# Kernel optimization log

Hardware: AMD Instinct MI355X
Metric: run time of the kernel (lower is better)

Reference implementation:

```python
import jax, jax.numpy as jnp
import numpy as np

N_FILTERS = 64
FILTER_SIZE = 64
N_FRAMES = 64
N_TO_KEEP = 128
MIN_SIZE = 512
N_SAMPLES = 32768
BATCH = 8


def pos_encoding(n_elements, n_sinusoids):
    t = np.linspace(1e-8, 1.0, n_elements)
    freq = np.linspace(1e-3, 1.0, n_sinusoids)
    return np.sin(t[:, None] * freq[None, :]).astype(np.float32)


def gammatone_filter_bank(n_filters, size, sr=22050.0):
    # 4th-order gammatone impulse responses, linearly spaced center freqs
    t = np.arange(size) / sr
    freqs = np.linspace(20.0, sr / 2 - 20.0, n_filters)
    b = 1.019 * 24.7 * (4.37 * freqs / 1000.0 + 1.0)  # ERB bandwidths
    g = (t[None, :] ** 3) * np.exp(-2 * np.pi * b[:, None] * t[None, :]) \
        * np.cos(2 * np.pi * freqs[:, None] * t[None, :])
    g = g / (np.abs(g).max(axis=-1, keepdims=True) + 1e-12)
    return g.astype(np.float32)


def setup_inputs() -> dict:
    key = jax.random.key(0)
    k1, k2 = jax.random.split(key)
    return {
        'target': jax.random.normal(k1, (BATCH, 1, N_SAMPLES), dtype=jnp.float32),
        'recon': jax.random.normal(k2, (BATCH, 1, N_SAMPLES), dtype=jnp.float32),
        'filters': jnp.asarray(gammatone_filter_bank(N_FILTERS, FILTER_SIZE)),
        'proj_time': jnp.asarray(pos_encoding(N_FRAMES, 128)),
        'proj_freq': jnp.asarray(pos_encoding(N_FILTERS, 128)),
    }


def fft_frequency_decompose(x, min_size):
    # band-limited octave decomposition: band of size s holds rfft bins [s/4, s/2)
    coeffs = jnp.fft.rfft(x, norm='ortho')
    n = x.shape[-1]
    bands = []
    start, end = 0, min_size // 2
    while end <= n // 2:
        spec = jnp.zeros(x.shape[:-1] + (end + 1,), dtype=coeffs.dtype)
        spec = spec.at[..., start:end].set(coeffs[..., start:end])
        bands.append(jnp.fft.irfft(spec, n=end * 2, norm='ortho'))
        start, end = end, end * 2
    return bands


def fft_convolve(a, b):
    n = a.shape[-1]
    pa = jnp.pad(a, [(0, 0)] * (a.ndim - 1) + [(0, n)])
    pb = jnp.pad(b, [(0, 0)] * (b.ndim - 1) + [(0, n)])
    spec = jnp.fft.rfft(pa) * jnp.fft.rfft(pb)  # broadcasts [B,1,.] x [1,F,.]
    return jnp.fft.irfft(spec, n=2 * n)[..., :n]


def max_pool1d(x, kernel, stride, pad):
    return jax.lax.reduce_window(
        x, -jnp.inf, jax.lax.max,
        (1, 1, kernel), (1, 1, stride),
        [(0, 0), (0, 0), (pad, pad)])


def sparsify2(x, k):
    # top-k over flattened (channels*time); pack events as value-scaled time
    # one-hots and binary channel one-hots
    b, c, t = x.shape
    flat = x.reshape(b, c * t)
    values, indices = jax.lax.top_k(flat, k)  # [b, k]
    ch, tm = indices // t, indices % t
    packed = (tm[..., None] == jnp.arange(t)[None, None, :]).astype(x.dtype) * values[..., None]  # [b,k,t]
    one_hot = (ch[..., None] == jnp.arange(c)[None, None, :]).astype(x.dtype)  # [b,k,c]
    return packed, one_hot


def _feature(x, filters, proj_time, proj_freq):
    bands = fft_frequency_decompose(x, MIN_SIZE)
    outs = []
    for band in bands:  # fixed small set of structurally distinct bands
        samples = band.shape[-1]
        filt = jnp.pad(filters[None, :, :], ((0, 0), (0, 0), (0, samples - FILTER_SIZE)))
        result = fft_convolve(band, filt)  # [B, n_filters, samples]
        stride = samples // 64
        pooled = max_pool1d(result, 2 * stride, stride, stride // 2)[..., :samples]  # [B, 64, 64]
        packed, one_hot = sparsify2(pooled, N_TO_KEEP)
        a = packed @ proj_time   # [B, k, 128]
        b = one_hot @ proj_freq  # [B, k, 128]
        outs.append(jnp.concatenate([a, b], axis=-1))
    return jnp.concatenate(outs, axis=-1)  # [B, k, 256 * n_bands]


def reference(target, recon, filters, proj_time, proj_freq):
    t = _feature(target, filters, proj_time, proj_freq)
    r = _feature(recon, filters, proj_time, proj_freq)
    return jnp.abs(t - r).mean()
```

## Files before the change

### kernel.cpp

```cpp
#include <hip/hip_runtime.h>
#include <hip/hip_bf16.h>

#define N_SAMP    32768
#define NBINS     16384
#define NSIG      16
#define NBANDS    7
#define K_TOP     128
#define BAND_STRIDE 65472

#define SST_F   0
#define SST_PT  4096
#define SST_PF  12288
#define SST_TOT 20480

#define TWO_PI 6.283185307179586f

typedef __attribute__((ext_vector_type(8))) short bf16x8;
typedef __attribute__((ext_vector_type(4))) float f32x4;

__device__ __forceinline__ float bf2f(__hip_bfloat16 v) { return __bfloat162float(v); }

__device__ __forceinline__ unsigned encf(float f) {
    unsigned u = __float_as_uint(f);
    return (u & 0x80000000u) ? ~u : (u | 0x80000000u);
}
__device__ __forceinline__ float decf(unsigned u) {
    return __uint_as_float((u & 0x80000000u) ? (u ^ 0x80000000u) : ~u);
}

__device__ __forceinline__ int band_M1sh(int b) { return b < 3 ? 4 : (b < 4 ? 5 : 6); }
__device__ __forceinline__ int band_Lsh(int b) {
    return b == 0 ? 5 : (b == 1 ? 6 : (b < 5 ? 7 : (b == 5 ? 8 : 9)));
}
__device__ __forceinline__ int band_M2sh(int b) {
    return b < 2 ? 4 : (b < 5 ? 5 : (b == 5 ? 6 : 7));
}

__global__ __launch_bounds__(256) void k_fwd1(
    const void* __restrict__ tgt, const void* __restrict__ rec,
    const void* __restrict__ f, const void* __restrict__ pt,
    const void* __restrict__ pf,
    __hip_bfloat16* __restrict__ staged,
    float* __restrict__ bands, float* __restrict__ accum,
    int* __restrict__ counter,
    float* __restrict__ T)
{
    const int tid   = threadIdx.x;
    const int sig   = blockIdx.y;

    if (blockIdx.x == 8) {
        float pv0 = bf2f(((const __hip_bfloat16*)tgt)[tid & 63]);
        int bad0 = (fabsf(pv0) > 1e8f) || (pv0 != pv0);
        const int isf = (__ballot(bad0) != 0ull);
        #pragma unroll
        for (int k = 0; k < 5; ++k) {
            int id = sig * 1280 + k * 256 + tid;
            const void* src; int idx;
            if (id < SST_PT)      { src = f;  idx = id; }
            else if (id < SST_PF) { src = pt; idx = id - SST_PT; }
            else                  { src = pf; idx = id - SST_PF; }
            float v = isf ? ((const float*)src)[idx]
                          : bf2f(((const __hip_bfloat16*)src)[idx]);
            staged[id] = __float2bfloat16(v);
        }
        for (int i = tid; i < 448; i += 256) {
            int g = i >> 6, j = i & 63;
            int off = 64 * g + 512 * ((1 << g) - 1);
            bands[(size_t)sig * BAND_STRIDE + off + j] = 0.f;
        }
        if (sig == 0 && tid == 0) { accum[0] = 0.f; counter[0] = 0; }
        return;
    }

    const int nbase = (blockIdx.x & 1) * 128;
    const int kgrp  = ((blockIdx.x >> 1) & 1) * 64;
    const int nqh   = (blockIdx.x >> 2) & 1;
    __shared__ __align__(16) __hip_bfloat16 xT[64][136];
    __shared__ float ct[128], st[128];
    __shared__ float2 t256[256];
    __shared__ float2 tF[128];

    {
        float sv, cv;
        sincosf(TWO_PI * (float)tid * (1.f / 256.f), &sv, &cv);
        t256[tid] = make_float2(cv, -sv);
        if (tid < 128) {
            sincosf(TWO_PI * (float)tid * (1.f / 128.f), &sv, &cv);
            ct[tid] = cv; st[tid] = sv;
            sincosf(TWO_PI * (float)tid * (1.f / 32768.f), &sv, &cv);
            tF[tid] = make_float2(cv, -sv);
        }
    }

    float pv = bf2f(((const __hip_bfloat16*)tgt)[tid & 63]);
    int bad = (fabsf(pv) > 1e8f) || (pv != pv);
    const int isf32 = (__ballot(bad) != 0ull);
    const void* xsrc = (sig < 8) ? tgt : rec;
    const int soff = (sig & 7) * N_SAMP;

    const int rloc = tid & 63;
    const int chb  = (tid >> 6) * 32;
    for (int c8 = 0; c8 < 32; c8 += 8) {
        union { bf16x8 v; __hip_bfloat16 h[8]; } u;
        #pragma unroll
        for (int uu = 0; uu < 8; ++uu) {
            int n1 = chb + c8 + uu;
            int gi = soff + n1 * 256 + nbase + nqh * 64 + rloc;
            float xv = isf32 ? ((const float*)xsrc)[gi]
                             : bf2f(((const __hip_bfloat16*)xsrc)[gi]);
            u.h[uu] = __float2bfloat16(xv);
        }
        *(bf16x8*)(&xT[rloc][chb + c8]) = u.v;
    }
    __syncthreads();

    const int tl = tid & 15, quad = (tid >> 4) & 3, w = tid >> 6;
    const int k1 = kgrp + w * 16 + tl;
    bf16x8 Arh[4], Arl[4], Aih[4], Ail[4];
    #pragma unroll
    for (int ki = 0; ki < 4; ++ki) {
        union { bf16x8 v; __hip_bfloat16 h[8]; } rh, rl, ih, il;
        #pragma unroll
        for (int j = 0; j < 8; ++j) {
            int n1 = ki * 32 + quad * 8 + j;
            int tt = (k1 * n1) & 127;
            float wre = ct[tt], wim = -st[tt];
            __hip_bfloat16 h1 = __float2bfloat16(wre);
            rh.h[j] = h1;
            rl.h[j] = __float2bfloat16(wre - bf2f(h1));
            __hip_bfloat16 h2 = __float2bfloat16(wim);
            ih.h[j] = h2;
            il.h[j] = __float2bfloat16(wim - bf2f(h2));
        }
        Arh[ki] = rh.v; Arl[ki] = rl.v; Aih[ki] = ih.v; Ail[ki] = il.v;
    }

    float2* To = (float2*)T + (size_t)sig * 128 * 256;
    const int mk = kgrp + w * 16 + quad * 4;
    for (int ni = 0; ni < 4; ++ni) {
        bf16x8 B[4];
        #pragma unroll
        for (int ki = 0; ki < 4; ++ki)
            B[ki] = *(const bf16x8*)(&xT[ni * 16 + tl][ki * 32 + quad * 8]);
        f32x4 aR = {0.f,0.f,0.f,0.f}, aI = {0.f,0.f,0.f,0.f};
        #pragma unroll
        for (int ki = 0; ki < 4; ++ki) {
            aR = __builtin_amdgcn_mfma_f32_16x16x32_bf16(Arh[ki], B[ki], aR, 0, 0, 0);
            aR = __builtin_amdgcn_mfma_f32_16x16x32_bf16(Arl[ki], B[ki], aR, 0, 0, 0);
            aI = __builtin_amdgcn_mfma_f32_16x16x32_bf16(Aih[ki], B[ki], aI, 0, 0, 0);
            aI = __builtin_amdgcn_mfma_f32_16x16x32_bf16(Ail[ki], B[ki], aI, 0, 0, 0);
        }
        const int n2 = nbase + nqh * 64 + ni * 16 + tl;
        #pragma unroll
        for (int rg = 0; rg < 4; ++rg) {
            int k1e = mk + rg;
            int m = k1e * n2;
            float2 e1 = t256[m >> 7];
            float2 e2 = tF[m & 127];
            float er = e1.x * e2.x - e1.y * e2.y;
            float ei = e1.x * e2.y + e1.y * e2.x;
            float Tr = aR[rg] * er - aI[rg] * ei;
            float Ti = aI[rg] * er + aR[rg] * ei;
            To[(size_t)k1e * 256 + n2] = make_float2(Tr, Ti);
        }
    }
}

__global__ __launch_bounds__(128) void k_fwd2(
    const float* __restrict__ T, float* __restrict__ C)
{
    const int k2  = threadIdx.x;
    const int k1  = blockIdx.x;
    const int sig = blockIdx.y;
    __shared__ float2 Ts[256];
    __shared__ float2 tw[256];
    const float2* Tin = (const float2*)T + ((size_t)sig * 128 + k1) * 256;
    for (int i = k2; i < 256; i += 128) Ts[i] = Tin[i];
    {
        float sv, cv;
        sincosf(TWO_PI * (float)k2 * (1.f / 256.f), &sv, &cv);
        tw[k2]       = make_float2(cv, -sv);
        tw[k2 + 128] = make_float2(-cv, sv);
    }
    __syncthreads();
    float er[4], ei[4];
    #pragma unroll
    for (int c = 0; c < 4; ++c) {
        float2 e = tw[(c * k2) & 255];
        er[c] = e.x; ei[c] = e.y;
    }
    float2 e4 = tw[(4 * k2) & 255];
    const float c4 = e4.x, s4 = e4.y;
    float Xr[4] = {0.f,0.f,0.f,0.f}, Xi[4] = {0.f,0.f,0.f,0.f};
    for (int n2 = 0; n2 < 256; n2 += 4) {
        #pragma unroll
        for (int c = 0; c < 4; ++c) {
            float2 t = Ts[n2 + c];
            Xr[c] += t.x * er[c] - t.y * ei[c];
            Xi[c] += t.x * ei[c] + t.y * er[c];
            float nr = er[c] * c4 - ei[c] * s4;
            ei[c]    = er[c] * s4 + ei[c] * c4;
            er[c] = nr;
        }
    }
    const float inv = 5.5242717280199030e-3f;
    float xr = (Xr[0] + Xr[1]) + (Xr[2] + Xr[3]);
    float xi = (Xi[0] + Xi[1]) + (Xi[2] + Xi[3]);
    float2* Co = (float2*)C + (size_t)sig * NBINS;
    Co[k1 + 128 * k2] = make_float2(xr * inv, xi * inv);
}

__global__ __launch_bounds__(256) void k_synthA(
    const float* __restrict__ C, float* __restrict__ G)
{
    const int tid = threadIdx.x;
    const int sig = blockIdx.y;
    const int bix = 63 - blockIdx.x;
    const int band = (bix == 0) ? 0 : (32 - __clz(bix));
    const int lbx  = (band == 0) ? 0 : (bix - (1 << (band - 1)));
    const int s    = 512 << band;
    const int m1sh = band_M1sh(band);
    const int lsh  = band_Lsh(band);
    const int m2sh = band_M2sh(band);
    const int M2   = 1 << m2sh;
    const int L    = 1 << lsh;
    const int L4   = L >> 2;
    const int a    = (band == 0) ? 0 : (128 << band);
    const int tix  = lbx * 256 + tid;
    const int j1lo = (lbx * 256) >> (lsh - 2);
    int j1cnt = 256 >> (lsh - 2);
    if (j1cnt > (1 << m1sh)) j1cnt = 1 << m1sh;
    __shared__ float2 Ds[256];
    const float2* D = (const float2*)C + (size_t)sig * NBINS + a;
    for (int i = tid; i < (j1cnt << m2sh); i += 256) {
        int j1o = i >> m2sh, j2 = i & (M2 - 1);
        Ds[i] = D[(j1lo + j1o) + (j2 << m1sh)];
    }
    __syncthreads();
    if (tix >= (128 << band)) return;
    const int j1o = (tix >> (lsh - 2)) - j1lo;
    const int m   = tix & (L4 - 1);
    const float2* Dj = Ds + (j1o << m2sh);
    float e0r = 1.f, e0i = 0.f, e1r, e1i, sr, si;
    sincosf(TWO_PI * (float)m / (float)L, &e1i, &e1r);
    sincosf(TWO_PI * (float)(2 * m) / (float)L, &si, &sr);
    float ar[4] = {0.f,0.f,0.f,0.f}, ai[4] = {0.f,0.f,0.f,0.f};
    for (int j2 = 0; j2 < M2; j2 += 4) {
        {   float2 d = Dj[j2];
            float tr = d.x * e0r - d.y * e0i, ti = d.x * e0i + d.y * e0r;
            ar[0] += tr; ai[0] += ti; ar[1] += tr; ai[1] += ti;
            ar[2] += tr; ai[2] += ti; ar[3] += tr; ai[3] += ti;
            float nr = e0r * sr - e0i * si; e0i = e0r * si + e0i * sr; e0r = nr;
        }
        {   float2 d = Dj[j2 + 1];
            float tr = d.x * e1r - d.y * e1i, ti = d.x * e1i + d.y * e1r;
            ar[0] += tr; ai[0] += ti;
            ar[1] -= ti; ai[1] += tr;
            ar[2] -= tr; ai[2] -= ti;
            ar[3] += ti; ai[3] -= tr;
            float nr = e1r * sr - e1i * si; e1i = e1r * si + e1i * sr; e1r = nr;
        }
        {   float2 d = Dj[j2 + 2];
            float tr = d.x * e0r - d.y * e0i, ti = d.x * e0i + d.y * e0r;
            ar[0] += tr; ai[0] += ti;
            ar[1] -= tr; ai[1] -= ti;
            ar[2] += tr; ai[2] += ti;
            ar[3] -= tr; ai[3] -= ti;
            float nr = e0r * sr - e0i * si; e0i = e0r * si + e0i * sr; e0r = nr;
        }
        {   float2 d = Dj[j2 + 3];
            float tr = d.x * e1r - d.y * e1i, ti = d.x * e1i + d.y * e1r;
            ar[0] += tr; ai[0] += ti;
            ar[1] += ti; ai[1] -= tr;
            ar[2] -= tr; ai[2] -= ti;
            ar[3] -= ti; ai[3] += tr;
            float nr = e1r * sr - e1i * si; e1i = e1r * si + e1i * sr; e1r = nr;
        }
    }
    const float sc = 2.f * rsqrtf((float)s);
    float2* Go = (float2*)G + (size_t)sig * 65024 + 512 * ((1 << band) - 1);
    const int base = ((tix >> (lsh - 2)) << lsh) + m;
    #pragma unroll
    for (int q = 0; q < 4; ++q)
        Go[base + q * L4] = make_float2(ar[q] * sc, ai[q] * sc);
}

__global__ __launch_bounds__(256) void k_synthB(
    const float* __restrict__ C, const float* __restrict__ G,
    float* __restrict__ bands)
{
    const int tid = threadIdx.x;
    const int sig = blockIdx.y;
    const int bix = 63 - blockIdx.x;
    const int band = (bix == 0) ? 0 : (32 - __clz(bix));
    const int lbx  = (band == 0) ? 0 : (bix - (1 << (band - 1)));
    const int s    = 512 << band;
    const int M1   = 1 << band_M1sh(band);
    const int lsh  = band_Lsh(band);
    const int n    = lbx * 256 + tid;
    const int s4   = s >> 2;
    if (n >= s4) return;
    const int m    = n & ((1 << lsh) - 1);
    const float2* Gi = (const float2*)G + (size_t)sig * 65024 + 512 * ((1 << band) - 1);
    float e0r = 1.f, e0i = 0.f, e1r, e1i, sr, si;
    sincosf(TWO_PI * (float)n / (float)s, &e1i, &e1r);
    sincosf(TWO_PI * (float)(2 * n) / (float)s, &si, &sr);
    float zr[4] = {0.f,0.f,0.f,0.f}, zi[4] = {0.f,0.f,0.f,0.f};
    for (int j1 = 0; j1 < M1; j1 += 4) {
        {   float2 g = Gi[((j1 + 0) << lsh) + m];
            float tr = g.x * e0r - g.y * e0i, ti = g.x * e0i + g.y * e0r;
            zr[0] += tr; zi[0] += ti; zr[1] += tr; zi[1] += ti;
            zr[2] += tr; zi[2] += ti; zr[3] += tr; zi[3] += ti;
            float nr = e0r * sr - e0i * si; e0i = e0r * si + e0i * sr; e0r = nr;
        }
        {   float2 g = Gi[((j1 + 1) << lsh) + m];
            float tr = g.x * e1r - g.y * e1i, ti = g.x * e1i + g.y * e1r;
            zr[0] += tr; zi[0] += ti;
            zr[1] -= ti; zi[1] += tr;
            zr[2] -= tr; zi[2] -= ti;
            zr[3] += ti; zi[3] -= tr;
            float nr = e1r * sr - e1i * si; e1i = e1r * si + e1i * sr; e1r = nr;
        }
        {   float2 g = Gi[((j1 + 2) << lsh) + m];
            float tr = g.x * e0r - g.y * e0i, ti = g.x * e0i + g.y * e0r;
            zr[0] += tr; zi[0] += ti;
            zr[1] -= tr; zi[1] -= ti;
            zr[2] += tr; zi[2] += ti;
            zr[3] -= tr; zi[3] -= ti;
            float nr = e0r * sr - e0i * si; e0i = e0r * si + e0i * sr; e0r = nr;
        }
        {   float2 g = Gi[((j1 + 3) << lsh) + m];
            float tr = g.x * e1r - g.y * e1i, ti = g.x * e1i + g.y * e1r;
            zr[0] += tr; zi[0] += ti;
            zr[1] += ti; zi[1] -= tr;
            zr[2] -= tr; zi[2] -= ti;
            zr[3] -= ti; zi[3] += tr;
            float nr = e1r * sr - e1i * si; e1i = e1r * si + e1i * sr; e1r = nr;
        }
    }
    const int poff = 64 * (band + 1) + 512 * ((1 << band) - 1);
    float* bo = bands + (size_t)sig * BAND_STRIDE + poff;
    if (band == 0) {
        const float dc = C[(size_t)sig * NBINS * 2] * 0.04419417382415922f;
        #pragma unroll
        for (int q = 0; q < 4; ++q) bo[n + q * s4] = zr[q] - dc;
    } else {
        #pragma unroll
        for (int q = 0; q < 4; ++q) {
            float val;
            switch (n & 3) {
                case 0:  val =  zr[q]; break;
                case 1:  val = -zi[q]; break;
                case 2:  val = -zr[q]; break;
                default: val =  zi[q]; break;
            }
            bo[n + q * s4] = val;
        }
    }
}

__global__ __launch_bounds__(256) void k_conv(
    const float* __restrict__ bands,
    const __hip_bfloat16* __restrict__ filters,
    float* __restrict__ segG)
{
    const int tid  = threadIdx.x;
    const int sig  = blockIdx.y;
    const int c    = blockIdx.x;
    const int band = 31 - __clz(c + 1);
    const int cidx = c + 1 - (1 << band);
    const int poff = 64 * (band + 1) + 512 * ((1 << band) - 1);
    const float* bp = bands + (size_t)sig * BAND_STRIDE + poff + cidx * 512;

    __shared__ __align__(16) __hip_bfloat16 xr[8][584];
    __shared__ float segP[64 * 4];

    if (tid < 72) {
        const int j = tid;
        const float* src = bp + 496 - 8 * j;
        float4 f0 = *(const float4*)(src + 12);
        float4 f1 = *(const float4*)(src + 8);
        float4 f2 = *(const float4*)(src + 4);
        float4 f3 = *(const float4*)(src + 0);
        __hip_bfloat16 w[16];
        w[0]  = __float2bfloat16(f0.w); w[1]  = __float2bfloat16(f0.z);
        w[2]  = __float2bfloat16(f0.y); w[3]  = __float2bfloat16(f0.x);
        w[4]  = __float2bfloat16(f1.w); w[5]  = __float2bfloat16(f1.z);
        w[6]  = __float2bfloat16(f1.y); w[7]  = __float2bfloat16(f1.x);
        w[8]  = __float2bfloat16(f2.w); w[9]  = __float2bfloat16(f2.z);
        w[10] = __float2bfloat16(f2.y); w[11] = __float2bfloat16(f2.x);
        w[12] = __float2bfloat16(f3.w); w[13] = __float2bfloat16(f3.z);
        w[14] = __float2bfloat16(f3.y); w[15] = __float2bfloat16(f3.x);
        #pragma unroll
        for (int p = 0; p < 8; ++p) {
            union { bf16x8 v; __hip_bfloat16 h[8]; } o;
            #pragma unroll
            for (int e = 0; e < 8; ++e) o.h[e] = w[p + e];
            *(bf16x8*)(&xr[p][8 * j]) = o.v;
        }
    }
    __syncthreads();

    const int tl   = tid & 15;
    const int quad = (tid >> 4) & 3;
    const int wave = tid >> 6;

    bf16x8 bf0[4], bf1[4];
    #pragma unroll
    for (int ft = 0; ft < 4; ++ft) {
        const __hip_bfloat16* fp = filters + ((ft * 16 + tl) * 64 + quad * 8);
        bf0[ft] = *(const bf16x8*)(fp);
        bf1[ft] = *(const bf16x8*)(fp + 32);
    }

    int s0 = 511 - wave * 128 - tl + 8 * quad;
    const __hip_bfloat16* xp = &xr[0][0] + (s0 & 7) * 584 + (s0 & ~7);

    const int spc = 512 >> (2 + band);
    float* segO = segG + (size_t)(sig * NBANDS + band) * 64 * 128 + cidx * spc;

    const float NEG = -3.4e38f;
    float run0 = NEG, run1 = NEG, run2 = NEG, run3 = NEG;
    const int per = (band >= 2) ? (1 << (band - 2)) : 1;

    for (int it = 0; it < 8; ++it) {
        const int t0 = wave * 128 + it * 16;
        bf16x8 a0 = *(const bf16x8*)(xp);
        bf16x8 a1 = *(const bf16x8*)(xp + 32);
        xp -= 16;
        f32x4 ac0 = {0.f,0.f,0.f,0.f}, ac1 = ac0, ac2 = ac0, ac3 = ac0;
        ac0 = __builtin_amdgcn_mfma_f32_16x16x32_bf16(a0, bf0[0], ac0, 0, 0, 0);
        ac0 = __builtin_amdgcn_mfma_f32_16x16x32_bf16(a1, bf1[0], ac0, 0, 0, 0);
        ac1 = __builtin_amdgcn_mfma_f32_16x16x32_bf16(a0, bf0[1], ac1, 0, 0, 0);
        ac1 = __builtin_amdgcn_mfma_f32_16x16x32_bf16(a1, bf1[1], ac1, 0, 0, 0);
        ac2 = __builtin_amdgcn_mfma_f32_16x16x32_bf16(a0, bf0[2], ac2, 0, 0, 0);
        ac2 = __builtin_amdgcn_mfma_f32_16x16x32_bf16(a1, bf1[2], ac2, 0, 0, 0);
        ac3 = __builtin_amdgcn_mfma_f32_16x16x32_bf16(a0, bf0[3], ac3, 0, 0, 0);
        ac3 = __builtin_amdgcn_mfma_f32_16x16x32_bf16(a1, bf1[3], ac3, 0, 0, 0);
        float m0 = fmaxf(fmaxf(ac0[0], ac0[1]), fmaxf(ac0[2], ac0[3]));
        float m1 = fmaxf(fmaxf(ac1[0], ac1[1]), fmaxf(ac1[2], ac1[3]));
        float m2 = fmaxf(fmaxf(ac2[0], ac2[1]), fmaxf(ac2[2], ac2[3]));
        float m3 = fmaxf(fmaxf(ac3[0], ac3[1]), fmaxf(ac3[2], ac3[3]));
        if (band == 0) {
            int sb = (t0 >> 2) + quad;
            segO[(tl     ) * 128 + sb] = m0;
            segO[(tl + 16) * 128 + sb] = m1;
            segO[(tl + 32) * 128 + sb] = m2;
            segO[(tl + 48) * 128 + sb] = m3;
        } else if (band == 1) {
            m0 = fmaxf(m0, __shfl_xor(m0, 16));
            m1 = fmaxf(m1, __shfl_xor(m1, 16));
            m2 = fmaxf(m2, __shfl_xor(m2, 16));
            m3 = fmaxf(m3, __shfl_xor(m3, 16));
            if ((quad & 1) == 0) {
                int sb = (t0 >> 3) + (quad >> 1);
                segO[(tl     ) * 128 + sb] = m0;
                segO[(tl + 16) * 128 + sb] = m1;
                segO[(tl + 32) * 128 + sb] = m2;
                segO[(tl + 48) * 128 + sb] = m3;
            }
        } else {
            m0 = fmaxf(m0, __shfl_xor(m0, 16)); m0 = fmaxf(m0, __shfl_xor(m0, 32));
            m1 = fmaxf(m1, __shfl_xor(m1, 16)); m1 = fmaxf(m1, __shfl_xor(m1, 32));
            m2 = fmaxf(m2, __shfl_xor(m2, 16)); m2 = fmaxf(m2, __shfl_xor(m2, 32));
            m3 = fmaxf(m3, __shfl_xor(m3, 16)); m3 = fmaxf(m3, __shfl_xor(m3, 32));
            run0 = fmaxf(run0, m0); run1 = fmaxf(run1, m1);
            run2 = fmaxf(run2, m2); run3 = fmaxf(run3, m3);
            if (((it + 1) & (per - 1)) == 0) {
                int sb = t0 >> (2 + band);
                float rv = quad == 0 ? run0 : quad == 1 ? run1
                         : quad == 2 ? run2 : run3;
                segO[(tl + 16 * quad) * 128 + sb] = rv;
                run0 = NEG; run1 = NEG; run2 = NEG; run3 = NEG;
            }
        }
    }
    if (band == 6) {
        float rv = quad == 0 ? run0 : quad == 1 ? run1
                 : quad == 2 ? run2 : run3;
        segP[(tl + 16 * quad) * 4 + wave] = rv;
        __syncthreads();
        if (tid < 128) {
            int f = tid & 63, sg = tid >> 6;
            segO[f * 128 + sg] =
                fmaxf(segP[f * 4 + 2 * sg], segP[f * 4 + 2 * sg + 1]);
        }
    }
}

__global__ __launch_bounds__(256) void k_topk(
    const float* __restrict__ segG,
    float* __restrict__ topv, int* __restrict__ topi)
{
    const int tid = threadIdx.x;
    const int band = blockIdx.x, sig = blockIdx.y;
    const float* segB = segG + (size_t)(sig * NBANDS + band) * 64 * 128;

    __shared__ unsigned hist[256];
    __shared__ unsigned scan[256];
    __shared__ unsigned long long list[512];
    __shared__ int sh_B, sh_nA, sh_cnt, sh_num;

    unsigned long long kk[16];
    #pragma unroll
    for (int q = 0; q < 16; ++q) {
        int i = q * 256 + tid;
        int f = i >> 6, t = i & 63;
        const float* sg = segB + f * 128;
        float m = fmaxf(sg[2 * t], sg[2 * t + 1]);
        if (t > 0)  m = fmaxf(m, sg[2 * t - 1]);
        if (t < 63) m = fmaxf(m, sg[2 * t + 2]);
        kk[q] = ((unsigned long long)encf(m) << 32) | (unsigned)(4095 - i);
    }

    int shift = 56;
    unsigned long long prefix = 0;
    int nA = 0;
    for (int lev = 0; lev < 8; ++lev) {
        hist[tid] = 0;
        __syncthreads();
        #pragma unroll
        for (int q = 0; q < 16; ++q) {
            bool inpre = (lev == 0) || ((kk[q] >> (shift + 8)) == prefix);
            if (inpre) atomicAdd(&hist[(unsigned)((kk[q] >> shift) & 255u)], 1u);
        }
        __syncthreads();
        scan[tid] = hist[tid];
        __syncthreads();
        for (int off = 1; off < 256; off <<= 1) {
            unsigned v = scan[tid] + ((tid + off < 256) ? scan[tid + off] : 0u);
            __syncthreads();
            scan[tid] = v;
            __syncthreads();
        }
        {
            unsigned ge = (unsigned)nA + scan[tid];
            unsigned gt = (unsigned)nA + ((tid < 255) ? scan[tid + 1] : 0u);
            if (ge >= 128u && gt < 128u) {
                sh_B = tid; sh_nA = (int)gt; sh_cnt = (int)hist[tid];
            }
        }
        __syncthreads();
        prefix = (prefix << 8) | (unsigned)sh_B;
        nA = sh_nA;
        if (nA + sh_cnt <= 511 || shift == 0) break;
        shift -= 8;
        __syncthreads();
    }

    list[tid] = 0ull; list[tid + 256] = 0ull;
    if (tid == 0) sh_num = 0;
    __syncthreads();
    #pragma unroll
    for (int q = 0; q < 16; ++q) {
        if ((kk[q] >> shift) >= prefix) {
            int p = atomicAdd(&sh_num, 1);
            if (p < 512) list[p] = kk[q];
        }
    }
    __syncthreads();

    for (int k = 2; k <= 512; k <<= 1) {
        for (int j = k >> 1; j > 0; j >>= 1) {
            for (int w = tid; w < 512; w += 256) {
                int l = w ^ j;
                if (l > w) {
                    unsigned long long av = list[w], bv = list[l];
                    bool up = ((w & k) == 0);
                    if ((av > bv) == up) { list[w] = bv; list[l] = av; }
                }
            }
            __syncthreads();
        }
    }
    if (tid < K_TOP) {
        unsigned long long key = list[511 - tid];
        const size_t ob = ((size_t)sig * NBANDS + band) * K_TOP + tid;
        topv[ob] = decf((unsigned)(key >> 32));
        topi[ob] = 4095 - (int)(key & 0xFFFFFFFFu);
    }
}

__global__ __launch_bounds__(256) void k_loss(
    const float* __restrict__ topv, const int* __restrict__ topi,
    const __hip_bfloat16* __restrict__ PT, const __hip_bfloat16* __restrict__ PF,
    float* __restrict__ accum, int* __restrict__ counter,
    unsigned* __restrict__ out)
{
    const int tid = threadIdx.x;
    const int band = blockIdx.x, b = blockIdx.y;
    const size_t bt = ((size_t)b * NBANDS + band) * K_TOP;
    const size_t br = ((size_t)(8 + b) * NBANDS + band) * K_TOP;
    __shared__ float vT[128], vR[128];
    __shared__ int   iT[128], iR[128];
    if (tid < 128) { vT[tid] = topv[bt + tid]; iT[tid] = topi[bt + tid]; }
    else { int j = tid - 128; vR[j] = topv[br + j]; iR[j] = topi[br + j]; }
    __syncthreads();
    float sum = 0.f;
    if (tid < 128) {
        #pragma unroll 4
        for (int k = 0; k < K_TOP; ++k) {
            float a = vT[k] * bf2f(PT[(iT[k] & 63) * 128 + tid]);
            float c = vR[k] * bf2f(PT[(iR[k] & 63) * 128 + tid]);
            sum += fabsf(a - c);
        }
    } else {
        const int j = tid - 128;
        #pragma unroll 4
        for (int k = 0; k < K_TOP; ++k) {
            float a = bf2f(PF[(iT[k] >> 6) * 128 + j]);
            float c = bf2f(PF[(iR[k] >> 6) * 128 + j]);
            sum += fabsf(a - c);
        }
    }
    __shared__ float red[256];
    __shared__ int amLast;
    red[tid] = sum;
    __syncthreads();
    for (int ofs = 128; ofs > 0; ofs >>= 1) {
        if (tid < ofs) red[tid] += red[tid + ofs];
        __syncthreads();
    }
    if (tid == 0) {
        atomicAdd(accum, red[0]);
        __threadfence();
        amLast = (atomicAdd(counter, 1) == NBANDS * 8 - 1);
    }
    __syncthreads();
    if (!amLast) return;
    if (tid == 0) {
        __threadfence();
        float L = atomicAdd(accum, 0.f) * (1.0f / 1835008.0f);
        unsigned lu = __float_as_uint(L);
        bool isnanL = ((lu & 0x7F800000u) == 0x7F800000u) && (lu & 0x007FFFFFu);
        float code;
        if      (isnanL)           code = 500.f;
        else if (L == 0.f)         code = 400.f;
        else if (fabsf(L) < 1e-6f) code = 600.f;
        else                       code = L;
        unsigned fb = __float_as_uint(code);
        unsigned hb = (fb + 0x7FFFu + ((fb >> 16) & 1u)) >> 16;
        out[0] = (hb << 16) | hb;
    }
}

extern "C" void kernel_launch(void* const* d_in, const int* in_sizes, int n_in,
                              void* d_out, int out_size, void* d_ws, size_t ws_size,
                              hipStream_t stream)
{
    float* C      = (float*)d_ws;
    float* bands  = C + (size_t)NSIG * NBINS * 2;
    float* segG   = bands + (size_t)NSIG * BAND_STRIDE;
    float* topv   = segG + (size_t)NSIG * NBANDS * 64 * 128;
    int*   topi   = (int*)(topv + (size_t)NSIG * NBANDS * K_TOP);
    float* accum  = (float*)(topi + (size_t)NSIG * NBANDS * K_TOP);
    int*   counter= (int*)(accum + 1);
    __hip_bfloat16* staged = (__hip_bfloat16*)(accum + 4);
    float* TG = (float*)(staged + SST_TOT);
    float* T  = TG;
    float* G  = TG;

    const __hip_bfloat16* fst = staged + SST_F;
    const __hip_bfloat16* pts = staged + SST_PT;
    const __hip_bfloat16* pfs = staged + SST_PF;

    k_fwd1   <<<dim3(9, NSIG),       256, 0, stream>>>(d_in[0], d_in[1],
                 d_in[2], d_in[3], d_in[4], staged, bands, accum, counter, T);
    k_fwd2   <<<dim3(128, NSIG),     128, 0, stream>>>(T, C);
    k_synthA <<<dim3(64, NSIG),      256, 0, stream>>>(C, G);
    k_synthB <<<dim3(64, NSIG),      256, 0, stream>>>(C, G, bands);
    k_conv   <<<dim3(127, NSIG),     256, 0, stream>>>(bands, fst, segG);
    k_topk   <<<dim3(NBANDS, NSIG),  256, 0, stream>>>(segG, topv, topi);
    k_loss   <<<dim3(NBANDS, 8),     256, 0, stream>>>(topv, topi, pts, pfs,
                 accum, counter, (unsigned*)d_out);
}
```

Baseline: 198.8 us.

## Fuse loss into top-k kernel via per-pair arrival counters, widen to 512 threads

Merges the k_loss kernel into k_topk. A per-(batch,band) atomic counter lets whichever of the target/recon blocks finishes second compute that pair's loss contribution, which removes one kernel launch and its dependency gap. The top-k block also grows from 256 to 512 threads, so each thread holds 8 keys instead of 16 and each bitonic stage needs one compare-exchange per thread instead of a loop. The cost is that half the threads sit idle in the histogram and scan phases, and the fused path depends on threadfence ordering for correctness.

```diff
diff --git a/kernel.cpp b/kernel.cpp
--- a/kernel.cpp
+++ b/kernel.cpp
@@ -42,7 +42,7 @@
     const void* __restrict__ pf,
     __hip_bfloat16* __restrict__ staged,
     float* __restrict__ bands, float* __restrict__ accum,
-    int* __restrict__ counter,
+    int* __restrict__ counter, int* __restrict__ lossCnt,
     float* __restrict__ T)
 {
     const int tid   = threadIdx.x;
@@ -68,7 +68,10 @@
             int off = 64 * g + 512 * ((1 << g) - 1);
             bands[(size_t)sig * BAND_STRIDE + off + j] = 0.f;
         }
-        if (sig == 0 && tid == 0) { accum[0] = 0.f; counter[0] = 0; }
+        if (sig == 0) {
+            if (tid == 0) { accum[0] = 0.f; counter[0] = 0; }
+            if (tid < 8 * NBANDS) lossCnt[tid] = 0;
+        }
         return;
     }
 
@@ -488,9 +491,12 @@
     }
 }
 
-__global__ __launch_bounds__(256) void k_topk(
+__global__ __launch_bounds__(512) void k_topk(
     const float* __restrict__ segG,
-    float* __restrict__ topv, int* __restrict__ topi)
+    float* __restrict__ topv, int* __restrict__ topi,
+    const __hip_bfloat16* __restrict__ PT, const __hip_bfloat16* __restrict__ PF,
+    int* __restrict__ lossCnt, float* __restrict__ accum,
+    int* __restrict__ counter, unsigned* __restrict__ out)
 {
     const int tid = threadIdx.x;
     const int band = blockIdx.x, sig = blockIdx.y;
@@ -499,12 +505,16 @@
     __shared__ unsigned hist[256];
     __shared__ unsigned scan[256];
     __shared__ unsigned long long list[512];
-    __shared__ int sh_B, sh_nA, sh_cnt, sh_num;
-
-    unsigned long long kk[16];
+    __shared__ int sh_B, sh_nA, sh_cnt, sh_num, sh_w2;
+    __shared__ float vT[128], vR[128];
+    __shared__ int   iT[128], iR[128];
+    __shared__ float red[256];
+    __shared__ int amLast;
+
+    unsigned long long kk[8];
     #pragma unroll
-    for (int q = 0; q < 16; ++q) {
-        int i = q * 256 + tid;
+    for (int q = 0; q < 8; ++q) {
+        int i = q * 512 + tid;
         int f = i >> 6, t = i & 63;
         const float* sg = segB + f * 128;
         float m = fmaxf(sg[2 * t], sg[2 * t + 1]);
@@ -517,23 +527,24 @@
     unsigned long long prefix = 0;
     int nA = 0;
     for (int lev = 0; lev < 8; ++lev) {
-        hist[tid] = 0;
+        if (tid < 256) hist[tid] = 0;
         __syncthreads();
         #pragma unroll
-        for (int q = 0; q < 16; ++q) {
+        for (int q = 0; q < 8; ++q) {
             bool inpre = (lev == 0) || ((kk[q] >> (shift + 8)) == prefix);
             if (inpre) atomicAdd(&hist[(unsigned)((kk[q] >> shift) & 255u)], 1u);
         }
         __syncthreads();
-        scan[tid] = hist[tid];
+        if (tid < 256) scan[tid] = hist[tid];
         __syncthreads();
         for (int off = 1; off < 256; off <<= 1) {
-            unsigned v = scan[tid] + ((tid + off < 256) ? scan[tid + off] : 0u);
+            unsigned v = 0;
+            if (tid < 256) v = scan[tid] + ((tid + off < 256) ? scan[tid + off] : 0u);
             __syncthreads();
-            scan[tid] = v;
+            if (tid < 256) scan[tid] = v;
             __syncthreads();
         }
-        {
+        if (tid < 256) {
             unsigned ge = (unsigned)nA + scan[tid];
             unsigned gt = (unsigned)nA + ((tid < 255) ? scan[tid + 1] : 0u);
             if (ge >= 128u && gt < 128u) {
@@ -548,11 +559,11 @@
         __syncthreads();
     }
 
-    list[tid] = 0ull; list[tid + 256] = 0ull;
+    if (tid < 256) { list[tid] = 0ull; list[tid + 256] = 0ull; }
     if (tid == 0) sh_num = 0;
     __syncthreads();
     #pragma unroll
-    for (int q = 0; q < 16; ++q) {
+    for (int q = 0; q < 8; ++q) {
         if ((kk[q] >> shift) >= prefix) {
             int p = atomicAdd(&sh_num, 1);
             if (p < 512) list[p] = kk[q];
@@ -562,13 +573,12 @@
 
     for (int k = 2; k <= 512; k <<= 1) {
         for (int j = k >> 1; j > 0; j >>= 1) {
-            for (int w = tid; w < 512; w += 256) {
-                int l = w ^ j;
-                if (l > w) {
-                    unsigned long long av = list[w], bv = list[l];
-                    bool up = ((w & k) == 0);
-                    if ((av > bv) == up) { list[w] = bv; list[l] = av; }
-                }
+            const int w = tid;
+            const int l = w ^ j;
+            if (l > w) {
+                unsigned long long av = list[w], bv = list[l];
+                bool up = ((w & k) == 0);
+                if ((av > bv) == up) { list[w] = bv; list[l] = av; }
             }
             __syncthreads();
         }
@@ -579,43 +589,42 @@
         topv[ob] = decf((unsigned)(key >> 32));
         topi[ob] = 4095 - (int)(key & 0xFFFFFFFFu);
     }
-}
-
-__global__ __launch_bounds__(256) void k_loss(
-    const float* __restrict__ topv, const int* __restrict__ topi,
-    const __hip_bfloat16* __restrict__ PT, const __hip_bfloat16* __restrict__ PF,
-    float* __restrict__ accum, int* __restrict__ counter,
-    unsigned* __restrict__ out)
-{
-    const int tid = threadIdx.x;
-    const int band = blockIdx.x, b = blockIdx.y;
+
+    __syncthreads();
+    if (tid == 0) {
+        __threadfence();
+        sh_w2 = (atomicAdd(&lossCnt[(sig & 7) * NBANDS + band], 1) == 1);
+    }
+    __syncthreads();
+    if (!sh_w2) return;
+    __threadfence();
+
+    const int b = sig & 7;
     const size_t bt = ((size_t)b * NBANDS + band) * K_TOP;
     const size_t br = ((size_t)(8 + b) * NBANDS + band) * K_TOP;
-    __shared__ float vT[128], vR[128];
-    __shared__ int   iT[128], iR[128];
     if (tid < 128) { vT[tid] = topv[bt + tid]; iT[tid] = topi[bt + tid]; }
-    else { int j = tid - 128; vR[j] = topv[br + j]; iR[j] = topi[br + j]; }
+    else if (tid < 256) {
+        int j = tid - 128; vR[j] = topv[br + j]; iR[j] = topi[br + j];
+    }
     __syncthreads();
     float sum = 0.f;
     if (tid < 128) {
         #pragma unroll 4
         for (int k = 0; k < K_TOP; ++k) {
             float a = vT[k] * bf2f(PT[(iT[k] & 63) * 128 + tid]);
-            float c = vR[k] * bf2f(PT[(iR[k] & 63) * 128 + tid]);
-            sum += fabsf(a - c);
-        }
-    } else {
+            float cc = vR[k] * bf2f(PT[(iR[k] & 63) * 128 + tid]);
+            sum += fabsf(a - cc);
+        }
+    } else if (tid < 256) {
         const int j = tid - 128;
         #pragma unroll 4
         for (int k = 0; k < K_TOP; ++k) {
             float a = bf2f(PF[(iT[k] >> 6) * 128 + j]);
-            float c = bf2f(PF[(iR[k] >> 6) * 128 + j]);
-            sum += fabsf(a - c);
-        }
-    }
-    __shared__ float red[256];
-    __shared__ int amLast;
-    red[tid] = sum;
+            float cc = bf2f(PF[(iR[k] >> 6) * 128 + j]);
+            sum += fabsf(a - cc);
+        }
+    }
+    if (tid < 256) red[tid] = sum;
     __syncthreads();
     for (int ofs = 128; ofs > 0; ofs >>= 1) {
         if (tid < ofs) red[tid] += red[tid + ofs];
@@ -655,7 +664,8 @@
     int*   topi   = (int*)(topv + (size_t)NSIG * NBANDS * K_TOP);
     float* accum  = (float*)(topi + (size_t)NSIG * NBANDS * K_TOP);
     int*   counter= (int*)(accum + 1);
-    __hip_bfloat16* staged = (__hip_bfloat16*)(accum + 4);
+    int*   lossCnt= (int*)(accum + 4);
+    __hip_bfloat16* staged = (__hip_bfloat16*)(accum + 64);
     float* TG = (float*)(staged + SST_TOT);
     float* T  = TG;
     float* G  = TG;
@@ -665,12 +675,12 @@
     const __hip_bfloat16* pfs = staged + SST_PF;
 
     k_fwd1   <<<dim3(9, NSIG),       256, 0, stream>>>(d_in[0], d_in[1],
-                 d_in[2], d_in[3], d_in[4], staged, bands, accum, counter, T);
+                 d_in[2], d_in[3], d_in[4], staged, bands, accum, counter,
+                 lossCnt, T);
     k_fwd2   <<<dim3(128, NSIG),     128, 0, stream>>>(T, C);
     k_synthA <<<dim3(64, NSIG),      256, 0, stream>>>(C, G);
     k_synthB <<<dim3(64, NSIG),      256, 0, stream>>>(C, G, bands);
     k_conv   <<<dim3(127, NSIG),     256, 0, stream>>>(bands, fst, segG);
-    k_topk   <<<dim3(NBANDS, NSIG),  256, 0, stream>>>(segG, topv, topi);
-    k_loss   <<<dim3(NBANDS, 8),     256, 0, stream>>>(topv, topi, pts, pfs,
-                 accum, counter, (unsigned*)d_out);
-}
+    k_topk   <<<dim3(NBANDS, NSIG),  512, 0, stream>>>(segG, topv, topi,
+                 pts, pfs, lossCnt, accum, counter, (unsigned*)d_out);
+}
```

Result: faster. 190.8 us (-4.0%).
